# Performance work log

Measured on AMD Instinct MI355X. Metric: run time of the kernel, lower is better.

Reference implementation:

```python
import jax, jax.numpy as jnp
import numpy as np

SCALE = 56          # descriptor spatial size (self.scale)
K_POS = 3           # positives: softmin over 3 nearest prototypes


def setup_inputs() -> dict:
    key = jax.random.key(0)
    k1, k2, k3 = jax.random.split(key, 3)
    B, DIM, H, W_ = 4, 1792, SCALE, SCALE
    P = 3136  # num_prototypes
    p = jax.random.normal(k1, (B, DIM, H, W_), dtype=jnp.float32)
    W = jax.random.normal(k2, (DIM, DIM), dtype=jnp.float32) * (1.0 / np.sqrt(DIM))
    b = jnp.zeros((DIM,), dtype=jnp.float32)
    C = jax.random.normal(k3, (DIM, P), dtype=jnp.float32) * (1.0 / np.sqrt(DIM))
    return {"p": p, "W": W, "b": b, "C": C}


def reference(p, W, b, C):
    B, DIM, H, Wd = p.shape
    # Descriptor: 1x1 conv (CoordConv2d without coords), no sigmoid, no avg-pool
    phi = jnp.einsum('bchw,dc->bdhw', p, W) + b[None, :, None, None]
    # b c h w -> b (h w) c
    phi_p = jnp.transpose(phi.reshape(B, DIM, H * Wd), (0, 2, 1))  # [B, HW, D]
    # squared-distance trick: ||a||^2 + ||c||^2 - 2 a.c
    features = jnp.sum(phi_p * phi_p, axis=2, keepdims=True)       # [B, HW, 1]
    centers = jnp.sum(C * C, axis=0, keepdims=True)                # [1, P]
    f_c = 2.0 * jnp.matmul(phi_p, C)                               # [B, HW, P]
    dist = jnp.sqrt(features + centers - f_c)                      # [B, HW, P]
    # k smallest distances (ascending)
    d = -jax.lax.top_k(-dist, K_POS)[0]                            # [B, HW, K]
    # softmin weight of the nearest prototype times its distance
    w0 = jax.nn.softmax(-d, axis=-1)[:, :, 0]
    score_flat = (w0 * d[:, :, 0])[:, :, None]                     # [B, HW, 1]
    # b (h w) c -> b c h w
    score = jnp.transpose(score_flat.reshape(B, H, Wd, 1), (0, 3, 1, 2))
    return score
```

## Files before the change

### kernel.cpp

```cpp
#include <hip/hip_runtime.h>
#include <hip/hip_bf16.h>
#include <cfloat>

#define BATCH 4
#define DIMC 1792
#define HWSZ 3136
#define NPROT 3136
#define NPAD 3200
#define MROWS 12544

typedef unsigned short u16;
typedef unsigned int u32;
using bf16x8 = __attribute__((ext_vector_type(8))) short;
using f32x4  = __attribute__((ext_vector_type(4))) float;

__device__ __forceinline__ float bf2f(u32 u) { return __uint_as_float(u << 16); }
__device__ __forceinline__ u16 f2bf(float x) {
    __hip_bfloat16 h = __float2bfloat16(x);
    return *reinterpret_cast<u16*>(&h);
}

__device__ __forceinline__ void gload_lds16(const u16* g, u16* l) {
    __builtin_amdgcn_global_load_lds(
        (const __attribute__((address_space(1))) void*)g,
        (__attribute__((address_space(3))) void*)l, 16, 0, 0);
}

__device__ __forceinline__ void ins3(float v, float& t0, float& t1, float& t2) {
    if (v < t2) {
        if (v < t1) {
            t2 = t1;
            if (v < t0) { t1 = t0; t0 = v; }
            else        { t1 = v; }
        } else {
            t2 = v;
        }
    }
}

__global__ void pack_p_kernel(const float* __restrict__ p, u16* __restrict__ Pbf) {
    __shared__ float tile[32][33];
    int hw0 = blockIdx.x * 32, c0 = blockIdx.y * 32, b = blockIdx.z;
    int tx = threadIdx.x, ty = threadIdx.y;
#pragma unroll
    for (int j = 0; j < 32; j += 8)
        tile[ty + j][tx] = p[((size_t)(b * DIMC + c0 + ty + j)) * HWSZ + hw0 + tx];
    __syncthreads();
#pragma unroll
    for (int j = 0; j < 32; j += 8) {
        int r = b * HWSZ + hw0 + ty + j;
        Pbf[(size_t)r * DIMC + c0 + tx] = f2bf(tile[tx][ty + j]);
    }
}

__global__ void pack_w_kernel(const float* __restrict__ W, u16* __restrict__ Wbf) {
    size_t i = (size_t)(blockIdx.x * 256 + threadIdx.x) * 4;
    float4 v = *(const float4*)(W + i);
    ushort4 o;
    o.x = f2bf(v.x); o.y = f2bf(v.y); o.z = f2bf(v.z); o.w = f2bf(v.w);
    *(ushort4*)(Wbf + i) = o;
}

__global__ void pack_c_kernel(const float* __restrict__ C, u16* __restrict__ CTbf) {
    __shared__ float tile[32][33];
    int j0 = blockIdx.x * 32, d0 = blockIdx.y * 32;
    int tx = threadIdx.x, ty = threadIdx.y;
#pragma unroll
    for (int jj = 0; jj < 32; jj += 8)
        tile[ty + jj][tx] = C[(size_t)(d0 + ty + jj) * NPROT + j0 + tx];
    __syncthreads();
#pragma unroll
    for (int jj = 0; jj < 32; jj += 8)
        CTbf[(size_t)(j0 + ty + jj) * DIMC + d0 + tx] = f2bf(tile[tx][ty + jj]);
}

__global__ void cn_kernel(const float* __restrict__ C, float* __restrict__ cn) {
    int j  = blockIdx.x * 256 + threadIdx.x;
    int d0 = blockIdx.y * 128;
    if (j >= NPROT) return;
    float s = 0.f;
    for (int d = d0; d < d0 + 128; ++d) {
        float v = C[(size_t)d * NPROT + j];
        s += v * v;
    }
    atomicAdd(&cn[j], s);
}

template<bool BIAS>
__global__ __launch_bounds__(256) void gemm_kernel(
    const u16* __restrict__ A,
    const u16* __restrict__ B,
    const float* __restrict__ bias,
    u16* __restrict__ out, int ldo)
{
    __shared__ __align__(16) u16 Als[128 * 32];
    __shared__ __align__(16) u16 Bls[128 * 32];
    const int tid  = threadIdx.x;
    const int wid  = tid >> 6;
    const int lane = tid & 63;
    const int r0 = blockIdx.x * 128;
    const int n0 = blockIdx.y * 128;

    const int srow = lane >> 2;
    const int sseg = (lane & 3) * 8;
    const u16* Ag = A + (size_t)(r0 + wid * 32 + srow) * DIMC + sseg;
    const u16* Bg = B + (size_t)(n0 + wid * 32 + srow) * DIMC + sseg;
    u16* AlsW = Als + wid * 1024;
    u16* BlsW = Bls + wid * 1024;

    const int wm = (wid >> 1) * 64;
    const int wn = (wid & 1) * 64;
    const int lrow = lane & 15;
    const int kseg = (lane >> 4) * 8;
    const int rsub = (lane >> 4) * 4;

    f32x4 acc[4][4];
#pragma unroll
    for (int m = 0; m < 4; ++m)
#pragma unroll
        for (int n = 0; n < 4; ++n)
            acc[m][n] = (f32x4){0.f, 0.f, 0.f, 0.f};

    for (int k0 = 0; k0 < DIMC; k0 += 32) {
        gload_lds16(Ag + k0,                      AlsW);
        gload_lds16(Ag + (size_t)16 * DIMC + k0,  AlsW + 512);
        gload_lds16(Bg + k0,                      BlsW);
        gload_lds16(Bg + (size_t)16 * DIMC + k0,  BlsW + 512);
        __syncthreads();
        bf16x8 af[4], bv[4];
#pragma unroll
        for (int m = 0; m < 4; ++m)
            af[m] = *(const bf16x8*)(Als + (wm + m * 16 + lrow) * 32 + kseg);
#pragma unroll
        for (int n = 0; n < 4; ++n)
            bv[n] = *(const bf16x8*)(Bls + (wn + n * 16 + lrow) * 32 + kseg);
#pragma unroll
        for (int m = 0; m < 4; ++m)
#pragma unroll
            for (int n = 0; n < 4; ++n)
                acc[m][n] = __builtin_amdgcn_mfma_f32_16x16x32_bf16(
                    af[m], bv[n], acc[m][n], 0, 0, 0);
        __syncthreads();
    }

#pragma unroll
    for (int n = 0; n < 4; ++n) {
        int col = n0 + wn + n * 16 + lrow;
        float bs = 0.f;
        if (BIAS) bs = bias[col];
#pragma unroll
        for (int m = 0; m < 4; ++m) {
            f32x4 v = acc[m][n];
#pragma unroll
            for (int i = 0; i < 4; ++i) {
                int row = r0 + wm + m * 16 + rsub + i;
                out[(size_t)row * ldo + col] = f2bf(v[i] + bs);
            }
        }
    }
}

__global__ void rn_kernel(const u16* __restrict__ phibf, float* __restrict__ rn) {
    int row  = blockIdx.x * 4 + (threadIdx.x >> 6);
    int lane = threadIdx.x & 63;
    const u16* pr = phibf + (size_t)row * DIMC;
    float s = 0.f;
#pragma unroll
    for (int it = 0; it < 7; ++it) {
        uint2 v = *(const uint2*)(pr + (it * 64 + lane) * 4);
        float f0 = bf2f(v.x & 0xffffu), f1 = bf2f(v.x >> 16);
        float f2 = bf2f(v.y & 0xffffu), f3 = bf2f(v.y >> 16);
        s += f0 * f0 + f1 * f1 + f2 * f2 + f3 * f3;
    }
#pragma unroll
    for (int off = 32; off > 0; off >>= 1) s += __shfl_down(s, off);
    if (lane == 0) rn[row] = s;
}

__global__ void top3_final_kernel(const u16* __restrict__ fc,
                                  const float* __restrict__ cn,
                                  const float* __restrict__ rn,
                                  float* __restrict__ out) {
    int row  = blockIdx.x * 4 + (threadIdx.x >> 6);
    int lane = threadIdx.x & 63;
    const u16* fr = fc + (size_t)row * NPAD;
    float t0 = FLT_MAX, t1 = FLT_MAX, t2 = FLT_MAX;
#pragma unroll
    for (int it = 0; it < 6; ++it) {
        int j0 = (it * 64 + lane) * 8;
        uint4 v = *(const uint4*)(fr + j0);
        u32 wd[4] = {v.x, v.y, v.z, v.w};
#pragma unroll
        for (int e = 0; e < 4; ++e) {
            float flo = bf2f(wd[e] & 0xffffu);
            float fhi = bf2f(wd[e] >> 16);
            ins3(cn[j0 + 2 * e]     - 2.f * flo, t0, t1, t2);
            ins3(cn[j0 + 2 * e + 1] - 2.f * fhi, t0, t1, t2);
        }
    }
    {
        int j = 3072 + lane;
        ins3(cn[j] - 2.f * bf2f((u32)fr[j]), t0, t1, t2);
    }
#pragma unroll
    for (int off = 32; off > 0; off >>= 1) {
        float s0 = __shfl_xor(t0, off);
        float s1 = __shfl_xor(t1, off);
        float s2 = __shfl_xor(t2, off);
        ins3(s0, t0, t1, t2);
        ins3(s1, t0, t1, t2);
        ins3(s2, t0, t1, t2);
    }
    if (lane == 0) {
        float rv = rn[row];
        float d0 = sqrtf(rv + t0), d1 = sqrtf(rv + t1), d2 = sqrtf(rv + t2);
        float w0 = 1.f / (1.f + expf(d0 - d1) + expf(d0 - d2));
        out[row] = w0 * d0;
    }
}

extern "C" void kernel_launch(void* const* d_in, const int* in_sizes, int n_in,
                              void* d_out, int out_size, void* d_ws, size_t ws_size,
                              hipStream_t stream) {
    const float* p    = (const float*)d_in[0];
    const float* W    = (const float*)d_in[1];
    const float* bias = (const float*)d_in[2];
    const float* C    = (const float*)d_in[3];
    float* out = (float*)d_out;

    char* w = (char*)d_ws;
    u16* Pbf   = (u16*)w;  w += (size_t)MROWS * DIMC * 2;
    u16* Wbf   = (u16*)w;  w += (size_t)DIMC * DIMC * 2;
    u16* CTbf  = (u16*)w;  w += (size_t)NPAD * DIMC * 2;
    u16* phibf = (u16*)w;  w += (size_t)MROWS * DIMC * 2;
    u16* fc    = (u16*)w;  w += (size_t)MROWS * NPAD * 2;
    float* cn  = (float*)w; w += (size_t)NPROT * 4;
    float* rn  = (float*)w;

    hipMemsetAsync(cn, 0, NPROT * sizeof(float), stream);

    pack_p_kernel<<<dim3(HWSZ / 32, DIMC / 32, BATCH), dim3(32, 8), 0, stream>>>(p, Pbf);
    pack_w_kernel<<<(DIMC * DIMC / 4) / 256, 256, 0, stream>>>(W, Wbf);
    pack_c_kernel<<<dim3(NPROT / 32, DIMC / 32), dim3(32, 8), 0, stream>>>(C, CTbf);
    cn_kernel<<<dim3((NPROT + 255) / 256, DIMC / 128), 256, 0, stream>>>(C, cn);

    gemm_kernel<true><<<dim3(MROWS / 128, DIMC / 128), 256, 0, stream>>>(
        Pbf, Wbf, bias, phibf, DIMC);
    rn_kernel<<<MROWS / 4, 256, 0, stream>>>(phibf, rn);
    gemm_kernel<false><<<dim3(MROWS / 128, NPAD / 128), 256, 0, stream>>>(
        phibf, CTbf, nullptr, fc, NPAD);
    top3_final_kernel<<<MROWS / 4, 256, 0, stream>>>(fc, cn, rn, out);
}
```

Before: 647.6 us.

## Fuse top-3 selection into distance GEMM epilogue and fold norms into producers

The second GEMM now does the per-row top-3 selection in its epilogue and writes small per-tile partial top-3 lists, so the large bf16 distance matrix is never written or read back. A small final kernel merges those partials and applies the softmin. Row norms are accumulated with atomics in the first GEMM's epilogue, and prototype norms are computed inside the C pack kernel, which removes the separate rn and cn kernels. The GEMMs also get an XCD-aware block swizzle, and the pack kernels write vectorized transposed stores. The cost is extra shuffle work and atomics in the GEMM epilogues.

```diff
diff --git a/kernel.cpp b/kernel.cpp
--- a/kernel.cpp
+++ b/kernel.cpp
@@ -8,6 +8,7 @@
 #define NPROT 3136
 #define NPAD 3200
 #define MROWS 12544
+#define NPT2 25
 
 typedef unsigned short u16;
 typedef unsigned int u32;
@@ -38,19 +39,30 @@
     }
 }
 
+__device__ __forceinline__ int xcd_swz(int bid, int nwg) {
+    int q = nwg >> 3, r = nwg & 7;
+    int xcd = bid & 7, idx = bid >> 3;
+    return (xcd < r ? xcd * (q + 1) : r * (q + 1) + (xcd - r) * q) + idx;
+}
+
 __global__ void pack_p_kernel(const float* __restrict__ p, u16* __restrict__ Pbf) {
     __shared__ float tile[32][33];
     int hw0 = blockIdx.x * 32, c0 = blockIdx.y * 32, b = blockIdx.z;
-    int tx = threadIdx.x, ty = threadIdx.y;
+    int tid = threadIdx.x;
+    int tx = tid & 31, ty = tid >> 5;
 #pragma unroll
     for (int j = 0; j < 32; j += 8)
         tile[ty + j][tx] = p[((size_t)(b * DIMC + c0 + ty + j)) * HWSZ + hw0 + tx];
     __syncthreads();
-#pragma unroll
-    for (int j = 0; j < 32; j += 8) {
-        int r = b * HWSZ + hw0 + ty + j;
-        Pbf[(size_t)r * DIMC + c0 + tx] = f2bf(tile[tx][ty + j]);
-    }
+    int hwl = tid >> 3;
+    int c4  = (tid & 7) * 4;
+    int r = b * HWSZ + hw0 + hwl;
+    ushort4 o;
+    o.x = f2bf(tile[c4 + 0][hwl]);
+    o.y = f2bf(tile[c4 + 1][hwl]);
+    o.z = f2bf(tile[c4 + 2][hwl]);
+    o.w = f2bf(tile[c4 + 3][hwl]);
+    *(ushort4*)(Pbf + (size_t)r * DIMC + c0 + c4) = o;
 }
 
 __global__ void pack_w_kernel(const float* __restrict__ W, u16* __restrict__ Wbf) {
@@ -61,45 +73,45 @@
     *(ushort4*)(Wbf + i) = o;
 }
 
-__global__ void pack_c_kernel(const float* __restrict__ C, u16* __restrict__ CTbf) {
+__global__ void pack_c_kernel(const float* __restrict__ C, u16* __restrict__ CTbf,
+                              float* __restrict__ cn) {
     __shared__ float tile[32][33];
     int j0 = blockIdx.x * 32, d0 = blockIdx.y * 32;
-    int tx = threadIdx.x, ty = threadIdx.y;
+    int tid = threadIdx.x;
+    int tx = tid & 31, ty = tid >> 5;
 #pragma unroll
     for (int jj = 0; jj < 32; jj += 8)
         tile[ty + jj][tx] = C[(size_t)(d0 + ty + jj) * NPROT + j0 + tx];
     __syncthreads();
-#pragma unroll
-    for (int jj = 0; jj < 32; jj += 8)
-        CTbf[(size_t)(j0 + ty + jj) * DIMC + d0 + tx] = f2bf(tile[tx][ty + jj]);
-}
-
-__global__ void cn_kernel(const float* __restrict__ C, float* __restrict__ cn) {
-    int j  = blockIdx.x * 256 + threadIdx.x;
-    int d0 = blockIdx.y * 128;
-    if (j >= NPROT) return;
+    int jl = tid >> 3;
+    int d4 = (tid & 7) * 4;
     float s = 0.f;
-    for (int d = d0; d < d0 + 128; ++d) {
-        float v = C[(size_t)d * NPROT + j];
-        s += v * v;
-    }
-    atomicAdd(&cn[j], s);
-}
-
-template<bool BIAS>
-__global__ __launch_bounds__(256) void gemm_kernel(
-    const u16* __restrict__ A,
-    const u16* __restrict__ B,
-    const float* __restrict__ bias,
-    u16* __restrict__ out, int ldo)
+    ushort4 o;
+    {
+        float f0 = tile[d4 + 0][jl], f1 = tile[d4 + 1][jl];
+        float f2 = tile[d4 + 2][jl], f3 = tile[d4 + 3][jl];
+        o.x = f2bf(f0); o.y = f2bf(f1); o.z = f2bf(f2); o.w = f2bf(f3);
+        s = f0 * f0 + f1 * f1 + f2 * f2 + f3 * f3;
+    }
+    *(ushort4*)(CTbf + (size_t)(j0 + jl) * DIMC + d0 + d4) = o;
+#pragma unroll
+    for (int off = 1; off < 8; off <<= 1) s += __shfl_xor(s, off);
+    if ((tid & 7) == 0) atomicAdd(&cn[j0 + jl], s);
+}
+
+__global__ __launch_bounds__(256) void gemm_bias_kernel(
+    const u16* __restrict__ A, const u16* __restrict__ B,
+    const float* __restrict__ bias, u16* __restrict__ out, int ldo, int nby,
+    float* __restrict__ rn)
 {
     __shared__ __align__(16) u16 Als[128 * 32];
     __shared__ __align__(16) u16 Bls[128 * 32];
     const int tid  = threadIdx.x;
     const int wid  = tid >> 6;
     const int lane = tid & 63;
-    const int r0 = blockIdx.x * 128;
-    const int n0 = blockIdx.y * 128;
+    const int swz = xcd_swz(blockIdx.x, gridDim.x);
+    const int r0 = (swz / nby) * 128;
+    const int n0 = (swz % nby) * 128;
 
     const int srow = lane >> 2;
     const int sseg = (lane & 3) * 8;
@@ -143,80 +155,147 @@
         __syncthreads();
     }
 
+    float bsv[4];
+#pragma unroll
+    for (int n = 0; n < 4; ++n) bsv[n] = bias[n0 + wn + n * 16 + lrow];
+#pragma unroll
+    for (int m = 0; m < 4; ++m) {
+        float rsum[4] = {0.f, 0.f, 0.f, 0.f};
+#pragma unroll
+        for (int n = 0; n < 4; ++n) {
+            int col = n0 + wn + n * 16 + lrow;
+            f32x4 v = acc[m][n];
+#pragma unroll
+            for (int i = 0; i < 4; ++i) {
+                float f = v[i] + bsv[n];
+                rsum[i] += f * f;
+                int row = r0 + wm + m * 16 + rsub + i;
+                out[(size_t)row * ldo + col] = f2bf(f);
+            }
+        }
+#pragma unroll
+        for (int i = 0; i < 4; ++i) {
+            float s = rsum[i];
+#pragma unroll
+            for (int off = 1; off < 16; off <<= 1) s += __shfl_xor(s, off);
+            if (lrow == 0)
+                atomicAdd(&rn[r0 + wm + m * 16 + rsub + i], s);
+        }
+    }
+}
+
+__global__ __launch_bounds__(256) void gemm_top3_kernel(
+    const u16* __restrict__ A, const u16* __restrict__ B,
+    const float* __restrict__ cn, float* __restrict__ ptop)
+{
+    __shared__ __align__(16) u16 Als[128 * 32];
+    __shared__ __align__(16) u16 Bls[128 * 32];
+    __shared__ float red[128][2][3];
+    const int tid  = threadIdx.x;
+    const int wid  = tid >> 6;
+    const int lane = tid & 63;
+    const int swz = xcd_swz(blockIdx.x, gridDim.x);
+    const int r0 = (swz / NPT2) * 128;
+    const int pt = swz % NPT2;
+    const int n0 = pt * 128;
+
+    const int srow = lane >> 2;
+    const int sseg = (lane & 3) * 8;
+    const u16* Ag = A + (size_t)(r0 + wid * 32 + srow) * DIMC + sseg;
+    const u16* Bg = B + (size_t)(n0 + wid * 32 + srow) * DIMC + sseg;
+    u16* AlsW = Als + wid * 1024;
+    u16* BlsW = Bls + wid * 1024;
+
+    const int wm = (wid >> 1) * 64;
+    const int wn = (wid & 1) * 64;
+    const int lrow = lane & 15;
+    const int kseg = (lane >> 4) * 8;
+    const int rsub = (lane >> 4) * 4;
+
+    f32x4 acc[4][4];
+#pragma unroll
+    for (int m = 0; m < 4; ++m)
+#pragma unroll
+        for (int n = 0; n < 4; ++n)
+            acc[m][n] = (f32x4){0.f, 0.f, 0.f, 0.f};
+
+    for (int k0 = 0; k0 < DIMC; k0 += 32) {
+        gload_lds16(Ag + k0,                      AlsW);
+        gload_lds16(Ag + (size_t)16 * DIMC + k0,  AlsW + 512);
+        gload_lds16(Bg + k0,                      BlsW);
+        gload_lds16(Bg + (size_t)16 * DIMC + k0,  BlsW + 512);
+        __syncthreads();
+        bf16x8 af[4], bv[4];
+#pragma unroll
+        for (int m = 0; m < 4; ++m)
+            af[m] = *(const bf16x8*)(Als + (wm + m * 16 + lrow) * 32 + kseg);
+#pragma unroll
+        for (int n = 0; n < 4; ++n)
+            bv[n] = *(const bf16x8*)(Bls + (wn + n * 16 + lrow) * 32 + kseg);
+#pragma unroll
+        for (int m = 0; m < 4; ++m)
+#pragma unroll
+            for (int n = 0; n < 4; ++n)
+                acc[m][n] = __builtin_amdgcn_mfma_f32_16x16x32_bf16(
+                    af[m], bv[n], acc[m][n], 0, 0, 0);
+        __syncthreads();
+    }
+
+    float cnv[4];
 #pragma unroll
     for (int n = 0; n < 4; ++n) {
         int col = n0 + wn + n * 16 + lrow;
-        float bs = 0.f;
-        if (BIAS) bs = bias[col];
-#pragma unroll
-        for (int m = 0; m < 4; ++m) {
-            f32x4 v = acc[m][n];
-#pragma unroll
-            for (int i = 0; i < 4; ++i) {
-                int row = r0 + wm + m * 16 + rsub + i;
-                out[(size_t)row * ldo + col] = f2bf(v[i] + bs);
+        cnv[n] = (col < NPROT) ? cn[col] : FLT_MAX;
+    }
+#pragma unroll
+    for (int m = 0; m < 4; ++m) {
+#pragma unroll
+        for (int i = 0; i < 4; ++i) {
+            float t0 = FLT_MAX, t1 = FLT_MAX, t2 = FLT_MAX;
+#pragma unroll
+            for (int n = 0; n < 4; ++n)
+                ins3(cnv[n] - 2.f * acc[m][n][i], t0, t1, t2);
+#pragma unroll
+            for (int off = 1; off < 16; off <<= 1) {
+                float s0 = __shfl_xor(t0, off);
+                float s1 = __shfl_xor(t1, off);
+                float s2 = __shfl_xor(t2, off);
+                ins3(s0, t0, t1, t2);
+                ins3(s1, t0, t1, t2);
+                ins3(s2, t0, t1, t2);
+            }
+            if (lrow == 0) {
+                int row = wm + m * 16 + rsub + i;
+                red[row][wid & 1][0] = t0;
+                red[row][wid & 1][1] = t1;
+                red[row][wid & 1][2] = t2;
             }
         }
     }
-}
-
-__global__ void rn_kernel(const u16* __restrict__ phibf, float* __restrict__ rn) {
-    int row  = blockIdx.x * 4 + (threadIdx.x >> 6);
-    int lane = threadIdx.x & 63;
-    const u16* pr = phibf + (size_t)row * DIMC;
-    float s = 0.f;
-#pragma unroll
-    for (int it = 0; it < 7; ++it) {
-        uint2 v = *(const uint2*)(pr + (it * 64 + lane) * 4);
-        float f0 = bf2f(v.x & 0xffffu), f1 = bf2f(v.x >> 16);
-        float f2 = bf2f(v.y & 0xffffu), f3 = bf2f(v.y >> 16);
-        s += f0 * f0 + f1 * f1 + f2 * f2 + f3 * f3;
-    }
-#pragma unroll
-    for (int off = 32; off > 0; off >>= 1) s += __shfl_down(s, off);
-    if (lane == 0) rn[row] = s;
-}
-
-__global__ void top3_final_kernel(const u16* __restrict__ fc,
-                                  const float* __restrict__ cn,
-                                  const float* __restrict__ rn,
-                                  float* __restrict__ out) {
-    int row  = blockIdx.x * 4 + (threadIdx.x >> 6);
-    int lane = threadIdx.x & 63;
-    const u16* fr = fc + (size_t)row * NPAD;
+    __syncthreads();
+    if (tid < 128) {
+        float t0 = red[tid][0][0], t1 = red[tid][0][1], t2 = red[tid][0][2];
+        ins3(red[tid][1][0], t0, t1, t2);
+        ins3(red[tid][1][1], t0, t1, t2);
+        ins3(red[tid][1][2], t0, t1, t2);
+        size_t base = ((size_t)(r0 + tid) * NPT2 + pt) * 3;
+        ptop[base + 0] = t0;
+        ptop[base + 1] = t1;
+        ptop[base + 2] = t2;
+    }
+}
+
+__global__ void final_kernel(const float* __restrict__ ptop,
+                             const float* __restrict__ rn,
+                             float* __restrict__ out) {
+    int r = blockIdx.x * 256 + threadIdx.x;
     float t0 = FLT_MAX, t1 = FLT_MAX, t2 = FLT_MAX;
-#pragma unroll
-    for (int it = 0; it < 6; ++it) {
-        int j0 = (it * 64 + lane) * 8;
-        uint4 v = *(const uint4*)(fr + j0);
-        u32 wd[4] = {v.x, v.y, v.z, v.w};
-#pragma unroll
-        for (int e = 0; e < 4; ++e) {
-            float flo = bf2f(wd[e] & 0xffffu);
-            float fhi = bf2f(wd[e] >> 16);
-            ins3(cn[j0 + 2 * e]     - 2.f * flo, t0, t1, t2);
-            ins3(cn[j0 + 2 * e + 1] - 2.f * fhi, t0, t1, t2);
-        }
-    }
-    {
-        int j = 3072 + lane;
-        ins3(cn[j] - 2.f * bf2f((u32)fr[j]), t0, t1, t2);
-    }
-#pragma unroll
-    for (int off = 32; off > 0; off >>= 1) {
-        float s0 = __shfl_xor(t0, off);
-        float s1 = __shfl_xor(t1, off);
-        float s2 = __shfl_xor(t2, off);
-        ins3(s0, t0, t1, t2);
-        ins3(s1, t0, t1, t2);
-        ins3(s2, t0, t1, t2);
-    }
-    if (lane == 0) {
-        float rv = rn[row];
-        float d0 = sqrtf(rv + t0), d1 = sqrtf(rv + t1), d2 = sqrtf(rv + t2);
-        float w0 = 1.f / (1.f + expf(d0 - d1) + expf(d0 - d2));
-        out[row] = w0 * d0;
-    }
+    const float* pp = ptop + (size_t)r * NPT2 * 3;
+    for (int q = 0; q < NPT2 * 3; ++q) ins3(pp[q], t0, t1, t2);
+    float rv = rn[r];
+    float d0 = sqrtf(rv + t0), d1 = sqrtf(rv + t1), d2 = sqrtf(rv + t2);
+    float w0 = 1.f / (1.f + expf(d0 - d1) + expf(d0 - d2));
+    out[r] = w0 * d0;
 }
 
 extern "C" void kernel_launch(void* const* d_in, const int* in_sizes, int n_in,
@@ -233,21 +312,19 @@
     u16* Wbf   = (u16*)w;  w += (size_t)DIMC * DIMC * 2;
     u16* CTbf  = (u16*)w;  w += (size_t)NPAD * DIMC * 2;
     u16* phibf = (u16*)w;  w += (size_t)MROWS * DIMC * 2;
-    u16* fc    = (u16*)w;  w += (size_t)MROWS * NPAD * 2;
+    float* ptop = (float*)w; w += (size_t)MROWS * NPT2 * 3 * 4;
     float* cn  = (float*)w; w += (size_t)NPROT * 4;
     float* rn  = (float*)w;
 
-    hipMemsetAsync(cn, 0, NPROT * sizeof(float), stream);
-
-    pack_p_kernel<<<dim3(HWSZ / 32, DIMC / 32, BATCH), dim3(32, 8), 0, stream>>>(p, Pbf);
+    hipMemsetAsync(cn, 0, (NPROT + MROWS) * sizeof(float), stream);
+
+    pack_p_kernel<<<dim3(HWSZ / 32, DIMC / 32, BATCH), 256, 0, stream>>>(p, Pbf);
     pack_w_kernel<<<(DIMC * DIMC / 4) / 256, 256, 0, stream>>>(W, Wbf);
-    pack_c_kernel<<<dim3(NPROT / 32, DIMC / 32), dim3(32, 8), 0, stream>>>(C, CTbf);
-    cn_kernel<<<dim3((NPROT + 255) / 256, DIMC / 128), 256, 0, stream>>>(C, cn);
-
-    gemm_kernel<true><<<dim3(MROWS / 128, DIMC / 128), 256, 0, stream>>>(
-        Pbf, Wbf, bias, phibf, DIMC);
-    rn_kernel<<<MROWS / 4, 256, 0, stream>>>(phibf, rn);
-    gemm_kernel<false><<<dim3(MROWS / 128, NPAD / 128), 256, 0, stream>>>(
-        phibf, CTbf, nullptr, fc, NPAD);
-    top3_final_kernel<<<MROWS / 4, 256, 0, stream>>>(fc, cn, rn, out);
-}
+    pack_c_kernel<<<dim3(NPROT / 32, DIMC / 32), 256, 0, stream>>>(C, CTbf, cn);
+
+    gemm_bias_kernel<<<(MROWS / 128) * (DIMC / 128), 256, 0, stream>>>(
+        Pbf, Wbf, bias, phibf, DIMC, DIMC / 128, rn);
+    gemm_top3_kernel<<<(MROWS / 128) * NPT2, 256, 0, stream>>>(
+        phibf, CTbf, cn, ptop);
+    final_kernel<<<MROWS / 256, 256, 0, stream>>>(ptop, rn, out);
+}
```

Result: slower. 801.8 us (+23.8%).
